# Performance work log

Measured on AMD Instinct MI355X. Metric: run time of the kernel, lower is better.

Reference implementation:

```python
import jax, jax.numpy as jnp
import numpy as np

B, S, D, H, L = 16, 1024, 512, 8, 32
DH = D // H  # 64


def setup_inputs() -> dict:
    key = jax.random.key(0)
    ks = jax.random.split(key, 12)
    p = lambda k, shape: 0.02 * jax.random.normal(k, shape, jnp.float32)
    return {
        "e_all": jax.random.normal(ks[0], (B, S, D), jnp.float32),
        "e_last": jax.random.normal(ks[1], (1, B, D), jnp.float32),
        "target": jax.random.normal(ks[2], (B, L, 3), jnp.float32),
        "Wq": p(ks[3], (D, D)), "bq": jnp.zeros((D,), jnp.float32),
        "Wk": p(ks[4], (D, D)), "bk": jnp.zeros((D,), jnp.float32),
        "Wv": p(ks[5], (D, D)), "bv": jnp.zeros((D,), jnp.float32),
        "Wo": p(ks[6], (D, D)), "bo": jnp.zeros((D,), jnp.float32),
        "W_ih": p(ks[7], (3 * D, 3 + D)), "W_hh": p(ks[8], (3 * D, D)),
        "b_ih": jnp.zeros((3 * D,), jnp.float32), "b_hh": jnp.zeros((3 * D,), jnp.float32),
        "W_out": p(ks[9], (3, D)), "b_out": jnp.zeros((3,), jnp.float32),
    }


def _forward(e_all, e_last, target, Wq, bq, Wk, bk, Wv, bv, Wo, bo,
             W_ih, W_hh, b_ih, b_hh, W_out, b_out):
    # K/V projections over e_all are loop-invariant in the original python loop;
    # hoist them (identical math). NOTE: the original reshape(B, H, S, DH) on a
    # [B, S, D] tensor is a plain row-major reshape (not a head split) -- kept faithful.
    K = (e_all @ Wk.T + bk).reshape(B, H, S, DH)
    V = (e_all @ Wv.T + bv).reshape(B, H, S, DH)
    h0 = e_last[0]  # [B, D] (single-layer GRU hidden)
    # teacher forcing: step 0 sees zeros, step i sees target[:, i-1]
    d_inputs = jnp.concatenate(
        [jnp.zeros((B, 1, 3), jnp.float32), target[:, :L - 1]], axis=1
    ).transpose(1, 0, 2)  # [L, B, 3]

    def step(h, d_in):
        q = (h @ Wq.T + bq).reshape(B, H, 1, DH)
        # faithful scaling quirk: dim_head ** 1 / 2 == DH / 2
        scores = jnp.einsum('bhqd,bhkd->bhqk', q, K) / (DH / 2)
        dist = jax.nn.softmax(scores, axis=-1)            # [B, H, 1, S]
        attn = jnp.einsum('bhqk,bhkd->bhqd', dist, V).reshape(B, D)
        attn = attn @ Wo.T + bo                           # out projection
        x = jnp.concatenate([attn, d_in], axis=-1)        # [B, D+3]
        gi = x @ W_ih.T + b_ih
        gh = h @ W_hh.T + b_hh
        i_r, i_z, i_n = jnp.split(gi, 3, axis=-1)
        h_r, h_z, h_n = jnp.split(gh, 3, axis=-1)
        r = jax.nn.sigmoid(i_r + h_r)
        z = jax.nn.sigmoid(i_z + h_z)
        n = jnp.tanh(i_n + r * h_n)
        h_new = (1 - z) * n + z * h
        out = h_new @ W_out.T + b_out                     # [B, 3]
        return h_new, (out, dist[:, :, 0, :])

    h_fin, (outs, dists) = jax.lax.scan(step, h0, d_inputs)
    d_outputs = outs.transpose(1, 0, 2)        # [B, L, 3]
    cross_attn = dists.transpose(1, 2, 0, 3)   # [B, H, L, S]
    return d_outputs, h_fin[None, :, :], cross_attn


def reference(e_all, e_last, target, Wq, bq, Wk, bk, Wv, bv, Wo, bo,
              W_ih, W_hh, b_ih, b_hh, W_out, b_out):
    return _forward(e_all, e_last, target, Wq, bq, Wk, bk, Wv, bv, Wo, bo,
                    W_ih, W_hh, b_ih, b_hh, W_out, b_out)
```

## Files before the change

### kernel.cpp

```cpp
#include <hip/hip_runtime.h>
#include <hip/hip_bf16.h>
#include <cstdint>

#define B_  16
#define S_  1024
#define D_  512
#define H_  8
#define L_  32
#define DH_ 64

typedef __attribute__((ext_vector_type(8))) short bf16x8;
typedef __attribute__((ext_vector_type(4))) float f32x4;

__device__ __forceinline__ float bf2f(unsigned short u) {
    union { unsigned int u; float f; } x; x.u = ((unsigned int)u) << 16; return x.f;
}
__device__ __forceinline__ unsigned short f2bf(float f) {
    union { float f; unsigned int u; } x; x.f = f;
    unsigned int r = x.u + 0x7fffu + ((x.u >> 16) & 1u);
    return (unsigned short)(r >> 16);
}

__device__ __forceinline__ void st_dev(float* p, float v) {
    __hip_atomic_store(p, v, __ATOMIC_RELAXED, __HIP_MEMORY_SCOPE_AGENT);
}
__device__ __forceinline__ float ld_dev(const float* p) {
    return __hip_atomic_load(p, __ATOMIC_RELAXED, __HIP_MEMORY_SCOPE_AGENT);
}


__global__ void k_conv(const float* __restrict__ in, unsigned short* __restrict__ out, int n) {
    int i = (blockIdx.x * 256 + threadIdx.x) * 4;
    int stride = gridDim.x * 1024;
    for (; i < n; i += stride) {
        float4 v = *reinterpret_cast<const float4*>(in + i);
        out[i + 0] = f2bf(v.x); out[i + 1] = f2bf(v.y);
        out[i + 2] = f2bf(v.z); out[i + 3] = f2bf(v.w);
    }
}

__global__ void k_transpose_bf(const float* __restrict__ in, unsigned short* __restrict__ out,
                               int R, int C) {
    __shared__ float tile[32][33];
    int c0 = blockIdx.x * 32, r0 = blockIdx.y * 32;
    int tx = threadIdx.x, ty = threadIdx.y;
#pragma unroll
    for (int i = 0; i < 4; i++)
        tile[ty + i * 8][tx] = in[(size_t)(r0 + ty + i * 8) * C + c0 + tx];
    __syncthreads();
#pragma unroll
    for (int i = 0; i < 4; i++)
        out[(size_t)(c0 + ty + i * 8) * R + r0 + tx] = f2bf(tile[tx][ty + i * 8]);
}

__global__ void k_conv_wih(const float* __restrict__ in, unsigned short* __restrict__ out) {
    int i = blockIdx.x * 256 + threadIdx.x;
    int j = i >> 9, k = i & 511;
    out[i] = f2bf(in[j * 515 + k]);
}

__global__ void k_bf_wd(const float* __restrict__ Wih, const float* __restrict__ bih,
                        const float* __restrict__ bo, float* __restrict__ bf_,
                        float* __restrict__ Wd) {
    int j = blockIdx.x * 256 + threadIdx.x;
    if (j >= 1536) return;
    float acc = bih[j];
    for (int k = 0; k < 512; k++) acc += Wih[(size_t)j * 515 + k] * bo[k];
    bf_[j] = acc;
    Wd[j * 3 + 0] = Wih[(size_t)j * 515 + 512];
    Wd[j * 3 + 1] = Wih[(size_t)j * 515 + 513];
    Wd[j * 3 + 2] = Wih[(size_t)j * 515 + 514];
}

__global__ void k_dterm2(const float* __restrict__ target, const float* __restrict__ Wd,
                         const float* __restrict__ bf_, const float* __restrict__ bhh,
                         float* __restrict__ gacc) {
    int i = blockIdx.x * 256 + threadIdx.x;
    int j = i % 3072; int bl = i / 3072; int b = bl % 16; int l = bl / 16;
    float acc;
    if (j < 1536) {
        acc = bf_[j];
        if (l > 0) {
            const float* tg = target + ((size_t)b * L_ + (l - 1)) * 3;
            acc += tg[0] * Wd[j * 3 + 0] + tg[1] * Wd[j * 3 + 1] + tg[2] * Wd[j * 3 + 2];
        }
    } else {
        acc = bhh[j - 1536];
    }
    gacc[i] = acc;
}

template <bool BF16OUT>
__global__ __launch_bounds__(256) void k_gemm_bt(
    const unsigned short* __restrict__ A, const unsigned short* __restrict__ Bm,
    void* __restrict__ Cout, const float* __restrict__ bias, int M, int N, int Kd) {
    __shared__ unsigned short As[128 * 64];
    __shared__ unsigned short Bs[128 * 64];
    const int t = threadIdx.x;
    const int lane = t & 63;
    const int w = t >> 6, wr = w >> 1, wc = w & 1;
    const int m0 = blockIdx.x * 128, n0 = blockIdx.y * 128;
    f32x4 acc[4][4];
#pragma unroll
    for (int i = 0; i < 4; i++)
#pragma unroll
        for (int j = 0; j < 4; j++) acc[i][j] = (f32x4){0.f, 0.f, 0.f, 0.f};

    const int rowt = t >> 3, colt = (t & 7) * 8;
    for (int k0 = 0; k0 < Kd; k0 += 64) {
#pragma unroll
        for (int i = 0; i < 4; i++) {
            int row = i * 32 + rowt;
            __builtin_amdgcn_global_load_lds(
                (const __attribute__((address_space(1))) unsigned int*)(A + (size_t)(m0 + row) * Kd + k0 + colt),
                (__attribute__((address_space(3))) unsigned int*)(As + (i * 256 + t) * 8), 16, 0, 0);
            __builtin_amdgcn_global_load_lds(
                (const __attribute__((address_space(1))) unsigned int*)(Bm + (size_t)(n0 + row) * Kd + k0 + colt),
                (__attribute__((address_space(3))) unsigned int*)(Bs + (i * 256 + t) * 8), 16, 0, 0);
        }
        asm volatile("s_waitcnt vmcnt(0)" ::: "memory");
        __syncthreads();
#pragma unroll
        for (int kk = 0; kk < 2; kk++) {
            bf16x8 af[4], bfr[4];
#pragma unroll
            for (int mi = 0; mi < 4; mi++)
                af[mi] = *reinterpret_cast<const bf16x8*>(
                    As + (wr * 64 + mi * 16 + (lane & 15)) * 64 + kk * 32 + (lane >> 4) * 8);
#pragma unroll
            for (int ni = 0; ni < 4; ni++)
                bfr[ni] = *reinterpret_cast<const bf16x8*>(
                    Bs + (wc * 64 + ni * 16 + (lane & 15)) * 64 + kk * 32 + (lane >> 4) * 8);
#pragma unroll
            for (int mi = 0; mi < 4; mi++)
#pragma unroll
                for (int ni = 0; ni < 4; ni++)
                    acc[mi][ni] = __builtin_amdgcn_mfma_f32_16x16x32_bf16(af[mi], bfr[ni], acc[mi][ni], 0, 0, 0);
        }
        __syncthreads();
    }
    const int rr = (lane >> 4) * 4, cc = lane & 15;
#pragma unroll
    for (int mi = 0; mi < 4; mi++) {
#pragma unroll
        for (int ni = 0; ni < 4; ni++) {
            int col = n0 + wc * 64 + ni * 16 + cc;
            float bv = bias ? bias[col] : 0.f;
            int rowb = m0 + wr * 64 + mi * 16 + rr;
#pragma unroll
            for (int r = 0; r < 4; r++) {
                float v = acc[mi][ni][r] + bv;
                if (BF16OUT) ((unsigned short*)Cout)[(size_t)(rowb + r) * N + col] = f2bf(v);
                else         ((float*)Cout)[(size_t)(rowb + r) * N + col] = v;
            }
        }
    }
}

__device__ __forceinline__ void group_barrier(unsigned* bar, unsigned tgt) {
    asm volatile("s_waitcnt vmcnt(0)" ::: "memory");
    __syncthreads();
    if (threadIdx.x == 0) {
        __hip_atomic_fetch_add(bar, 1u, __ATOMIC_RELAXED, __HIP_MEMORY_SCOPE_AGENT);
        while (__hip_atomic_load(bar, __ATOMIC_RELAXED, __HIP_MEMORY_SCOPE_AGENT) < tgt)
            __builtin_amdgcn_s_sleep(1);
    }
    __syncthreads();
}

__global__ __launch_bounds__(1024, 1) void k_decode(
    const unsigned short* __restrict__ K16, const unsigned short* __restrict__ V16,
    const unsigned short* __restrict__ Wq16, const float* __restrict__ bq,
    const unsigned short* __restrict__ Wf16, const unsigned short* __restrict__ Whh16,
    const float* __restrict__ gacc, float* __restrict__ pvP, float* __restrict__ ssAll,
    float* __restrict__ hnewB, const float* __restrict__ e_last,
    const float* __restrict__ Wout, const float* __restrict__ bout,
    float* __restrict__ dout, float* __restrict__ hfin, float* __restrict__ cross,
    unsigned* __restrict__ bars) {
    const int t = threadIdx.x, lane = t & 63, w = t >> 6;
    const int bi = blockIdx.x >> 4, hd = (blockIdx.x >> 1) & 7, sh = blockIdx.x & 1;
    const int p = blockIdx.x & 15;

    __shared__ char Ks[65536];
    __shared__ char Vs[65536];
    __shared__ float hsh[512];
    __shared__ float qsh[64];
    __shared__ float esh[512];
    __shared__ float red[1024];
    __shared__ float pvred[1024];
    __shared__ float ash2[512];
    __shared__ float gsh[192];
    __shared__ float wred[32];
    __shared__ float invs[8];

    const size_t base = (size_t)bi * (S_ * D_) + (size_t)hd * (S_ * DH_) + (size_t)sh * (512 * 64);

    {
        const int row = t >> 1, half = t & 1;
        const unsigned short* kr = K16 + base + (size_t)row * 64 + half * 32;
        const unsigned short* vr = V16 + base + (size_t)row * 64 + half * 32;
        char* krow = Ks + row * 128;
        char* vrow = Vs + row * 128;
#pragma unroll
        for (int c = 0; c < 4; c++) {
            int slot = half * 4 + c;
            *reinterpret_cast<bf16x8*>(krow + ((slot ^ (row & 7)) * 16)) =
                *reinterpret_cast<const bf16x8*>(kr + c * 8);
            *reinterpret_cast<bf16x8*>(vrow + ((slot ^ (row & 7)) * 16)) =
                *reinterpret_cast<const bf16x8*>(vr + c * 8);
        }
    }
    if (t < 512) hsh[t] = e_last[bi * 512 + t];

    bf16x8 wq[4];
    {
        const unsigned short* wrow = Wq16 + (size_t)(hd * 64 + (t & 63)) * 512 + (t >> 6) * 32;
#pragma unroll
        for (int i = 0; i < 4; i++) wq[i] = *reinterpret_cast<const bf16x8*>(wrow + i * 8);
    }
    __syncthreads();

    for (int l = 0; l < L_; l++) {
        {
            const float* xk = hsh + (t >> 6) * 32;
            float qa = 0.f;
#pragma unroll
            for (int kk = 0; kk < 4; kk++)
#pragma unroll
                for (int e = 0; e < 8; e++)
                    qa += xk[kk * 8 + e] * bf2f((unsigned short)wq[kk][e]);
            red[t] = qa;
        }
        __syncthreads();
        if (t < 64) {
            float s = bq[hd * 64 + t];
#pragma unroll
            for (int pp = 0; pp < 16; pp++) s += red[pp * 64 + t];
            qsh[t] = s * (1.f / 32.f);
        }
        __syncthreads();

        {
            const int r = t & 511, kp = t >> 9;
            const char* krow = Ks + r * 128;
            float sc = 0.f;
#pragma unroll
            for (int c = 0; c < 4; c++) {
                int slot = kp * 4 + c;
                bf16x8 kv = *reinterpret_cast<const bf16x8*>(krow + ((slot ^ (r & 7)) * 16));
#pragma unroll
                for (int e = 0; e < 8; e++)
                    sc += qsh[slot * 8 + e] * bf2f((unsigned short)kv[e]);
            }
            red[t] = sc;
        }
        __syncthreads();
        if (t < 512) {
            float e = __expf(red[t] + red[t + 512]);
            esh[t] = e;
            cross[((size_t)(bi * 8 + hd) * 32 + l) * 1024 + sh * 512 + t] = e;
            float wsum = e;
#pragma unroll
            for (int off = 1; off < 64; off <<= 1) wsum += __shfl_xor(wsum, off);
            if (lane == 0) wred[w] = wsum;
        }
        __syncthreads();
        if (t == 0) {
            float s = 0.f;
#pragma unroll
            for (int i = 0; i < 8; i++) s += wred[i];
            st_dev(ssAll + ((size_t)l * 16 + bi) * 16 + p, s);
        }

        {
            const int o = lane & 7, sr8 = lane >> 3;
            float acc[8];
#pragma unroll
            for (int e2 = 0; e2 < 8; e2++) acc[e2] = 0.f;
#pragma unroll
            for (int i = 0; i < 4; i++) {
                int r = w * 32 + sr8 + 8 * i;
                bf16x8 vv = *reinterpret_cast<const bf16x8*>(Vs + r * 128 + ((o ^ (r & 7)) * 16));
                float ev = esh[r];
#pragma unroll
                for (int e2 = 0; e2 < 8; e2++)
                    acc[e2] += ev * bf2f((unsigned short)vv[e2]);
            }
#pragma unroll
            for (int off = 8; off < 64; off <<= 1)
#pragma unroll
                for (int e2 = 0; e2 < 8; e2++)
                    acc[e2] += __shfl_xor(acc[e2], off);
            if (lane < 8) {
#pragma unroll
                for (int e2 = 0; e2 < 8; e2++)
                    pvred[w * 64 + lane * 8 + e2] = acc[e2];
            }
        }
        __syncthreads();
        if (t < 64) {
            float s = 0.f;
#pragma unroll
            for (int w2 = 0; w2 < 16; w2++) s += pvred[w2 * 64 + t];
            st_dev(pvP + ((size_t)(bi * 16 + p)) * 64 + t, s);
        }

        group_barrier(bars + bi * 64 + 2 * l, 16u);

        if (t < 16) wred[t] = ld_dev(ssAll + ((size_t)l * 16 + bi) * 16 + t);
        __syncthreads();
        if (t < 8) invs[t] = 1.f / (wred[2 * t] + wred[2 * t + 1]);
        __syncthreads();
        if (t < 512) {
            int h2 = t >> 6, kk = t & 63;
            const float* pvb = pvP + ((size_t)(bi * 16 + h2 * 2)) * 64 + kk;
            ash2[t] = (ld_dev(pvb) + ld_dev(pvb + 64)) * invs[h2];
        }
        __syncthreads();
        if (t < 768) {
            const int o = t >> 3, kp = t & 7;
            const int c = o >> 5, dl = o & 31;
            const int j = c * 512 + p * 32 + dl;
            const unsigned short* wfr = Wf16 + (size_t)j * 512 + kp * 64;
            const unsigned short* whr = Whh16 + (size_t)j * 512 + kp * 64;
            float gi = 0.f, gh = 0.f;
#pragma unroll
            for (int kk2 = 0; kk2 < 8; kk2++) {
                bf16x8 wv = *reinterpret_cast<const bf16x8*>(wfr + kk2 * 8);
                bf16x8 hv = *reinterpret_cast<const bf16x8*>(whr + kk2 * 8);
#pragma unroll
                for (int e = 0; e < 8; e++) {
                    gi += ash2[kp * 64 + kk2 * 8 + e] * bf2f((unsigned short)wv[e]);
                    gh += hsh[kp * 64 + kk2 * 8 + e] * bf2f((unsigned short)hv[e]);
                }
            }
            red[t] = gi;
            pvred[t] = gh;
        }
        __syncthreads();
        if (t < 96) {
            const int c = t >> 5, dl = t & 31;
            const int j = c * 512 + p * 32 + dl;
            const float* gb = gacc + ((size_t)l * 16 + bi) * 3072;
            float gi = gb[j], gh = gb[1536 + j];
#pragma unroll
            for (int q = 0; q < 8; q++) { gi += red[t * 8 + q]; gh += pvred[t * 8 + q]; }
            gsh[t] = gi;
            gsh[96 + t] = gh;
        }
        __syncthreads();
        if (t < 32) {
            const int d = p * 32 + t;
            float gir = gsh[t], giz = gsh[32 + t], gin = gsh[64 + t];
            float ghr = gsh[96 + t], ghz = gsh[128 + t], ghn = gsh[160 + t];
            float r = 1.f / (1.f + __expf(-(gir + ghr)));
            float z = 1.f / (1.f + __expf(-(giz + ghz)));
            float n = tanhf(gin + r * ghn);
            float hnew = (1.f - z) * n + z * hsh[d];
            st_dev(hnewB + bi * 512 + d, hnew);
        }

        group_barrier(bars + bi * 64 + 2 * l + 1, 16u);

        if (t < 512) hsh[t] = ld_dev(hnewB + bi * 512 + t);
        __syncthreads();

        if (p == 0) {
            if (t < 512) {
                float hv = hsh[t];
                float p0 = hv * Wout[t], p1 = hv * Wout[512 + t], p2 = hv * Wout[1024 + t];
#pragma unroll
                for (int off = 1; off < 64; off <<= 1) {
                    p0 += __shfl_xor(p0, off);
                    p1 += __shfl_xor(p1, off);
                    p2 += __shfl_xor(p2, off);
                }
                if (lane == 0) { wred[w * 3] = p0; wred[w * 3 + 1] = p1; wred[w * 3 + 2] = p2; }
            }
            __syncthreads();
            if (t < 3) {
                float s = 0.f;
#pragma unroll
                for (int i = 0; i < 8; i++) s += wred[i * 3 + t];
                dout[((size_t)bi * 32 + l) * 3 + t] = s + bout[t];
            }
        }
    }
    if (p == 0 && t < 512) hfin[bi * 512 + t] = hsh[t];
}

__global__ void k_norm(float* __restrict__ cross, const float* __restrict__ ssAll) {
    int i = blockIdx.x * 256 + threadIdx.x;
    size_t b4 = (size_t)i * 4;
    int bhl = (int)(b4 >> 10);
    int l = bhl & 31, hd = (bhl >> 5) & 7, bi = bhl >> 8;
    const float* sp = ssAll + ((size_t)l * 16 + bi) * 16 + hd * 2;
    float inv = 1.f / (sp[0] + sp[1]);
    float4 v = *reinterpret_cast<float4*>(cross + b4);
    v.x *= inv; v.y *= inv; v.z *= inv; v.w *= inv;
    *reinterpret_cast<float4*>(cross + b4) = v;
}

extern "C" void kernel_launch(void* const* d_in, const int* in_sizes, int n_in,
                              void* d_out, int out_size, void* d_ws, size_t ws_size,
                              hipStream_t stream) {
    (void)in_sizes; (void)n_in; (void)out_size; (void)ws_size;
    const float* e_all  = (const float*)d_in[0];
    const float* e_last = (const float*)d_in[1];
    const float* target = (const float*)d_in[2];
    const float* Wq     = (const float*)d_in[3];
    const float* bq     = (const float*)d_in[4];
    const float* Wk     = (const float*)d_in[5];
    const float* bk     = (const float*)d_in[6];
    const float* Wv     = (const float*)d_in[7];
    const float* bv     = (const float*)d_in[8];
    const float* Wo     = (const float*)d_in[9];
    const float* bo     = (const float*)d_in[10];
    const float* W_ih   = (const float*)d_in[11];
    const float* W_hh   = (const float*)d_in[12];
    const float* b_ih   = (const float*)d_in[13];
    const float* b_hh   = (const float*)d_in[14];
    const float* W_out  = (const float*)d_in[15];
    const float* b_out  = (const float*)d_in[16];
    float* out = (float*)d_out;

    char* ws = (char*)d_ws;
    size_t off = 0;
    auto alloc = [&](size_t bytes) -> void* {
        void* p = ws + off; off += (bytes + 255) & ~(size_t)255; return p;
    };
    unsigned short* eA    = (unsigned short*)alloc(16777216);
    unsigned short* K16   = (unsigned short*)alloc(16777216);
    unsigned short* V16   = (unsigned short*)alloc(16777216);
    unsigned short* Wk16  = (unsigned short*)alloc(524288);
    unsigned short* Wv16  = (unsigned short*)alloc(524288);
    unsigned short* Wq16  = (unsigned short*)alloc(524288);
    unsigned short* Whh16 = (unsigned short*)alloc(1572864);
    unsigned short* Wih16 = (unsigned short*)alloc(1572864);
    unsigned short* WoT   = (unsigned short*)alloc(524288);
    unsigned short* Wf16  = (unsigned short*)alloc(1572864);
    float* Wf32  = (float*)alloc(3145728);
    float* bf_   = (float*)alloc(6144);
    float* Wd    = (float*)alloc(18432);
    float* gacc  = (float*)alloc(6291456);
    float* pvP   = (float*)alloc(65536);
    float* ssAll = (float*)alloc(32768);
    float* hnewB = (float*)alloc(32768);
    unsigned* bars = (unsigned*)alloc(4096);

    float* d_outputs = out;
    float* h_fin     = out + 1536;
    float* cross     = out + 9728;

    hipMemsetAsync(bars, 0, 4096, stream);
    k_conv<<<2048, 256, 0, stream>>>(e_all, eA, 8388608);
    k_conv<<<256, 256, 0, stream>>>(Wk, Wk16, 262144);
    k_conv<<<256, 256, 0, stream>>>(Wv, Wv16, 262144);
    k_conv<<<256, 256, 0, stream>>>(Wq, Wq16, 262144);
    k_conv<<<768, 256, 0, stream>>>(W_hh, Whh16, 786432);
    k_transpose_bf<<<dim3(16, 16), dim3(32, 8), 0, stream>>>(Wo, WoT, 512, 512);
    k_conv_wih<<<3072, 256, 0, stream>>>(W_ih, Wih16);
    k_bf_wd<<<6, 256, 0, stream>>>(W_ih, b_ih, bo, bf_, Wd);
    k_dterm2<<<6144, 256, 0, stream>>>(target, Wd, bf_, b_hh, gacc);
    k_gemm_bt<true><<<dim3(128, 4), 256, 0, stream>>>(eA, Wk16, K16, bk, 16384, 512, 512);
    k_gemm_bt<true><<<dim3(128, 4), 256, 0, stream>>>(eA, Wv16, V16, bv, 16384, 512, 512);
    k_gemm_bt<false><<<dim3(12, 4), 256, 0, stream>>>(Wih16, WoT, Wf32, nullptr, 1536, 512, 512);
    k_conv<<<768, 256, 0, stream>>>(Wf32, Wf16, 786432);

    k_decode<<<256, 1024, 0, stream>>>(K16, V16, Wq16, bq, Wf16, Whh16, gacc, pvP, ssAll,
                                       hnewB, e_last, W_out, b_out, d_outputs, h_fin,
                                       cross, bars);

    k_norm<<<4096, 256, 0, stream>>>(cross, ssAll);
}
```

Baseline: 752.1 us.

## Hoist W_hh gate matvec before group barrier and pad shared vectors

Moves the h·W_hh gate computation so it runs before the first inter-block group barrier, since it depends only on the previous hidden state, letting it overlap the barrier wait instead of sitting on the critical path after it. Replaces the shared-memory partial reduction and its extra __syncthreads with 8-lane shuffle reductions, and adds the gacc bias directly in the gate-update threads. Uses padded copies of h and the attention vector (stride 66) to reduce LDS bank conflicts. Costs some extra shared memory and a second copy of h per step.

After: 714.3 us. 5.0% less time.

```diff
diff --git a/kernel.cpp b/kernel.cpp
--- a/kernel.cpp
+++ b/kernel.cpp
@@ -184,12 +184,14 @@
     __shared__ char Ks[65536];
     __shared__ char Vs[65536];
     __shared__ float hsh[512];
+    __shared__ float hshp[528];
+    __shared__ float ashp[528];
     __shared__ float qsh[64];
     __shared__ float esh[512];
     __shared__ float red[1024];
     __shared__ float pvred[1024];
-    __shared__ float ash2[512];
-    __shared__ float gsh[192];
+    __shared__ float gish[96];
+    __shared__ float ghsh[96];
     __shared__ float wred[32];
     __shared__ float invs[8];
 
@@ -210,7 +212,11 @@
                 *reinterpret_cast<const bf16x8*>(vr + c * 8);
         }
     }
-    if (t < 512) hsh[t] = e_last[bi * 512 + t];
+    if (t < 512) {
+        float hv = e_last[bi * 512 + t];
+        hsh[t] = hv;
+        hshp[(t >> 6) * 66 + (t & 63)] = hv;
+    }
 
     bf16x8 wq[4];
     {
@@ -305,6 +311,26 @@
             st_dev(pvP + ((size_t)(bi * 16 + p)) * 64 + t, s);
         }
 
+        if (t < 768) {
+            const int o = t >> 3, kp = t & 7;
+            const int c = o >> 5, dl = o & 31;
+            const int j = c * 512 + p * 32 + dl;
+            const unsigned short* whr = Whh16 + (size_t)j * 512 + kp * 64;
+            const float* x = hshp + kp * 66;
+            float gh = 0.f;
+#pragma unroll
+            for (int kk2 = 0; kk2 < 8; kk2++) {
+                bf16x8 hv = *reinterpret_cast<const bf16x8*>(whr + kk2 * 8);
+#pragma unroll
+                for (int e = 0; e < 8; e++)
+                    gh += x[kk2 * 8 + e] * bf2f((unsigned short)hv[e]);
+            }
+            gh += __shfl_xor(gh, 1);
+            gh += __shfl_xor(gh, 2);
+            gh += __shfl_xor(gh, 4);
+            if ((t & 7) == 0) ghsh[o] = gh;
+        }
+
         group_barrier(bars + bi * 64 + 2 * l, 16u);
 
         if (t < 16) wred[t] = ld_dev(ssAll + ((size_t)l * 16 + bi) * 16 + t);
@@ -314,7 +340,7 @@
         if (t < 512) {
             int h2 = t >> 6, kk = t & 63;
             const float* pvb = pvP + ((size_t)(bi * 16 + h2 * 2)) * 64 + kk;
-            ash2[t] = (ld_dev(pvb) + ld_dev(pvb + 64)) * invs[h2];
+            ashp[h2 * 66 + kk] = (ld_dev(pvb) + ld_dev(pvb + 64)) * invs[h2];
         }
         __syncthreads();
         if (t < 768) {
@@ -322,37 +348,30 @@
             const int c = o >> 5, dl = o & 31;
             const int j = c * 512 + p * 32 + dl;
             const unsigned short* wfr = Wf16 + (size_t)j * 512 + kp * 64;
-            const unsigned short* whr = Whh16 + (size_t)j * 512 + kp * 64;
-            float gi = 0.f, gh = 0.f;
+            const float* x = ashp + kp * 66;
+            float gi = 0.f;
 #pragma unroll
             for (int kk2 = 0; kk2 < 8; kk2++) {
                 bf16x8 wv = *reinterpret_cast<const bf16x8*>(wfr + kk2 * 8);
-                bf16x8 hv = *reinterpret_cast<const bf16x8*>(whr + kk2 * 8);
-#pragma unroll
-                for (int e = 0; e < 8; e++) {
-                    gi += ash2[kp * 64 + kk2 * 8 + e] * bf2f((unsigned short)wv[e]);
-                    gh += hsh[kp * 64 + kk2 * 8 + e] * bf2f((unsigned short)hv[e]);
-                }
-            }
-            red[t] = gi;
-            pvred[t] = gh;
-        }
-        __syncthreads();
-        if (t < 96) {
-            const int c = t >> 5, dl = t & 31;
-            const int j = c * 512 + p * 32 + dl;
-            const float* gb = gacc + ((size_t)l * 16 + bi) * 3072;
-            float gi = gb[j], gh = gb[1536 + j];
-#pragma unroll
-            for (int q = 0; q < 8; q++) { gi += red[t * 8 + q]; gh += pvred[t * 8 + q]; }
-            gsh[t] = gi;
-            gsh[96 + t] = gh;
+#pragma unroll
+                for (int e = 0; e < 8; e++)
+                    gi += x[kk2 * 8 + e] * bf2f((unsigned short)wv[e]);
+            }
+            gi += __shfl_xor(gi, 1);
+            gi += __shfl_xor(gi, 2);
+            gi += __shfl_xor(gi, 4);
+            if ((t & 7) == 0) gish[o] = gi;
         }
         __syncthreads();
         if (t < 32) {
             const int d = p * 32 + t;
-            float gir = gsh[t], giz = gsh[32 + t], gin = gsh[64 + t];
-            float ghr = gsh[96 + t], ghz = gsh[128 + t], ghn = gsh[160 + t];
+            const float* gb = gacc + ((size_t)l * 16 + bi) * 3072;
+            float gir = gish[t]      + gb[d];
+            float giz = gish[32 + t] + gb[512 + d];
+            float gin = gish[64 + t] + gb[1024 + d];
+            float ghr = ghsh[t]      + gb[1536 + d];
+            float ghz = ghsh[32 + t] + gb[2048 + d];
+            float ghn = ghsh[64 + t] + gb[2560 + d];
             float r = 1.f / (1.f + __expf(-(gir + ghr)));
             float z = 1.f / (1.f + __expf(-(giz + ghz)));
             float n = tanhf(gin + r * ghn);
@@ -362,7 +381,11 @@
 
         group_barrier(bars + bi * 64 + 2 * l + 1, 16u);
 
-        if (t < 512) hsh[t] = ld_dev(hnewB + bi * 512 + t);
+        if (t < 512) {
+            float hv = ld_dev(hnewB + bi * 512 + t);
+            hsh[t] = hv;
+            hshp[(t >> 6) * 66 + (t & 63)] = hv;
+        }
         __syncthreads();
 
         if (p == 0) {
```
